# Kernel optimization log

Measured on AMD Instinct MI355X. Metric: run time of the kernel, lower is better.

Reference implementation:

```python
import jax, jax.numpy as jnp
import numpy as np

N = 100000
C = 20
D = 2001
REG = 0.001


def setup_inputs() -> dict:
    key = jax.random.key(0)
    k1, k2, k3, k4 = jax.random.split(key, 4)
    weights = jax.random.normal(k1, (C, D), dtype=jnp.float32)
    X = jax.random.normal(k2, (N, D), dtype=jnp.float32)
    Y = jax.random.randint(k3, (N,), 0, C, dtype=jnp.int64)
    init_weights = jax.random.uniform(k4, (C, D), dtype=jnp.float32)
    return {"weights": weights, "X": X, "Y": Y, "init_weights": init_weights}


def reference(weights, X, Y, init_weights):
    # scores[i, c] = X[i] . weights[c]  -> one batched GEMM [N,D]x[D,C]
    scores = jnp.einsum('nd,cd->nc', X, weights)
    # matmul(weights[Y[i]], X[i]) = scores[i, Y[i]]
    picked = jnp.take_along_axis(scores, Y[:, None].astype(jnp.int32), axis=1)[:, 0]  # [N]
    # logsumexp over classes of -X[i].weights (stable, single pass)
    lse = jax.nn.logsumexp(-scores, axis=1)  # [N]
    data_loss = jnp.mean(picked + lse)
    # torch.norm(self.weights, 2) on a matrix = Frobenius norm of init_weights (constant wrt input weights)
    reg = REG * jnp.sqrt(jnp.sum(init_weights * init_weights))
    return data_loss + reg
```

## Files before the change

kernel.cpp:

```cpp
#include <hip/hip_runtime.h>
#include <math.h>

#define DD 2001
#define CC 20
#define NN 100000
#define REGC 0.001f

__device__ __forceinline__ float4 ld4(const float* p) {
  return *reinterpret_cast<const float4*>(p);
}

template <int STRD, int STRC>
__global__ __launch_bounds__(64) void loss_main(
    const float* __restrict__ X,
    const float* __restrict__ Wp,
    const int* __restrict__ Y,
    float* __restrict__ out) {
  const float* W = (const float*)__builtin_assume_aligned(Wp, 64);
  const int lane = threadIdx.x;
  const int row0 = blockIdx.x * 64 + lane;
  const bool valid = row0 < NN;
  const int row = valid ? row0 : (NN - 1);
  const float* xr = X + (size_t)row * DD;

  float acc[CC];
#pragma unroll
  for (int c = 0; c < CC; ++c) acc[c] = 0.f;

  float4 c0 = ld4(xr), c1 = ld4(xr + 4), c2 = ld4(xr + 8), c3 = ld4(xr + 12);
#pragma unroll 1
  for (int k = 0; k < 125; ++k) {
    float4 n0 = {0, 0, 0, 0}, n1 = {0, 0, 0, 0}, n2 = {0, 0, 0, 0}, n3 = {0, 0, 0, 0};
    if (k < 124) {
      const float* p = xr + (k + 1) * 16;
      n0 = ld4(p); n1 = ld4(p + 4); n2 = ld4(p + 8); n3 = ld4(p + 12);
    }
    const int dbase = k * 16;
#pragma unroll
    for (int j = 0; j < 4; ++j) {
      const float4 x = (j == 0) ? c0 : (j == 1) ? c1 : (j == 2) ? c2 : c3;
      const int d0 = dbase + j * 4;
#pragma unroll
      for (int c = 0; c < CC; ++c) {
        float a = acc[c];
        a = fmaf(x.x, W[(d0 + 0) * STRD + c * STRC], a);
        a = fmaf(x.y, W[(d0 + 1) * STRD + c * STRC], a);
        a = fmaf(x.z, W[(d0 + 2) * STRD + c * STRC], a);
        a = fmaf(x.w, W[(d0 + 3) * STRD + c * STRC], a);
        acc[c] = a;
      }
    }
    c0 = n0; c1 = n1; c2 = n2; c3 = n3;
  }
  {
    const float x = xr[DD - 1];
#pragma unroll
    for (int c = 0; c < CC; ++c)
      acc[c] = fmaf(x, W[(DD - 1) * STRD + c * STRC], acc[c]);
  }

  float mx = -3.402823466e38f;
#pragma unroll
  for (int c = 0; c < CC; ++c) mx = fmaxf(mx, -acc[c]);
  float s = 0.f;
#pragma unroll
  for (int c = 0; c < CC; ++c) s += __expf(-acc[c] - mx);
  const int y = valid ? Y[row] : 0;
  float picked = 0.f;
#pragma unroll
  for (int c = 0; c < CC; ++c) picked = (c == y) ? acc[c] : picked;
  float li = picked + mx + __logf(s);
  li = valid ? li : 0.f;

#pragma unroll
  for (int off = 32; off > 0; off >>= 1) li += __shfl_xor(li, off, 64);
  if (lane == 0) atomicAdd(out, li * (1.0f / NN));
}

__global__ void reg_kernel(const float* __restrict__ IW, float* __restrict__ out) {
  __shared__ float red[256];
  float s = 0.f;
  for (int i = threadIdx.x; i < CC * DD; i += 256) {
    float v = IW[i];
    s += v * v;
  }
  red[threadIdx.x] = s;
  __syncthreads();
  for (int w = 128; w > 0; w >>= 1) {
    if (threadIdx.x < w) red[threadIdx.x] += red[threadIdx.x + w];
    __syncthreads();
  }
  if (threadIdx.x == 0) out[0] = REGC * sqrtf(red[0]);
}

__global__ void transpose_w(const float* __restrict__ W, float* __restrict__ Wt) {
  int i = blockIdx.x * 256 + threadIdx.x;
  if (i < CC * DD) {
    int c = i / DD;
    int d = i - c * DD;
    Wt[d * CC + c] = W[i];
  }
}

extern "C" void kernel_launch(void* const* d_in, const int* in_sizes, int n_in,
                              void* d_out, int out_size, void* d_ws, size_t ws_size,
                              hipStream_t stream) {
  const float* W  = (const float*)d_in[0];
  const float* X  = (const float*)d_in[1];
  const int*   Y  = (const int*)d_in[2];
  const float* IW = (const float*)d_in[3];
  float* out = (float*)d_out;

  reg_kernel<<<1, 256, 0, stream>>>(IW, out);

  const int nblocks = (NN + 63) / 64;
  if (ws_size >= (size_t)(CC * DD) * sizeof(float)) {
    float* Wt = (float*)d_ws;
    transpose_w<<<(CC * DD + 255) / 256, 256, 0, stream>>>(W, Wt);
    loss_main<CC, 1><<<nblocks, 64, 0, stream>>>(X, Wt, Y, out);
  } else {
    loss_main<1, DD><<<nblocks, 64, 0, stream>>>(X, W, Y, out);
  }
}
```

Measured before the change: 1.215 ms.

## Stage X tiles through LDS with coalesced loads and double-buffered registers

Each wavefront now loads 64-column chunks of its 64 rows cooperatively, with 16 lanes per row reading contiguous float4s. It writes them into a padded LDS tile so each lane can then read its own row's chunk for the per-class FMAs. The next chunk is prefetched into a second register buffer while the current one is consumed. The goal is to replace the old strided per-row global loads, which coalesced poorly, with coalesced transfers. The cost is LDS traffic, possible LDS hazards between write and read within the wave, and heavy register use from the 32 float4 buffers. The workspace-size fallback path is removed.

```diff
diff --git a/kernel.cpp b/kernel.cpp
--- a/kernel.cpp
+++ b/kernel.cpp
@@ -6,57 +6,88 @@
 #define NN 100000
 #define REGC 0.001f
 
+#define CH 64
+#define NFULL 31
+#define DTAIL 1984
+#define RSTR 68
+
 __device__ __forceinline__ float4 ld4(const float* p) {
   return *reinterpret_cast<const float4*>(p);
 }
 
-template <int STRD, int STRC>
 __global__ __launch_bounds__(64) void loss_main(
     const float* __restrict__ X,
-    const float* __restrict__ Wp,
+    const float* __restrict__ Wt,
     const int* __restrict__ Y,
     float* __restrict__ out) {
-  const float* W = (const float*)__builtin_assume_aligned(Wp, 64);
+  __shared__ float xs[64 * RSTR];
   const int lane = threadIdx.x;
-  const int row0 = blockIdx.x * 64 + lane;
-  const bool valid = row0 < NN;
-  const int row = valid ? row0 : (NN - 1);
-  const float* xr = X + (size_t)row * DD;
+  const int rowbase = blockIdx.x * 64;
+
+  const int myrow0 = rowbase + lane;
+  const bool valid = myrow0 < NN;
+  const int myrow = valid ? myrow0 : NN - 1;
+
+  const int srow = lane >> 4;
+  const int sf   = lane & 15;
 
   float acc[CC];
 #pragma unroll
   for (int c = 0; c < CC; ++c) acc[c] = 0.f;
 
-  float4 c0 = ld4(xr), c1 = ld4(xr + 4), c2 = ld4(xr + 8), c3 = ld4(xr + 12);
-#pragma unroll 1
-  for (int k = 0; k < 125; ++k) {
-    float4 n0 = {0, 0, 0, 0}, n1 = {0, 0, 0, 0}, n2 = {0, 0, 0, 0}, n3 = {0, 0, 0, 0};
-    if (k < 124) {
-      const float* p = xr + (k + 1) * 16;
-      n0 = ld4(p); n1 = ld4(p + 4); n2 = ld4(p + 8); n3 = ld4(p + 12);
+  float4 va[16], vb[16];
+
+  size_t sbase[16];
+#pragma unroll
+  for (int q = 0; q < 16; ++q) {
+    int r = rowbase + q * 4 + srow;
+    r = r < NN ? r : NN - 1;
+    sbase[q] = (size_t)r * DD + sf * 4;
+  }
+
+#pragma unroll
+  for (int q = 0; q < 16; ++q) va[q] = ld4(X + sbase[q]);
+
+  auto body = [&](float4 (&cur)[16], float4 (&nxt)[16], int k) {
+#pragma unroll
+    for (int q = 0; q < 16; ++q)
+      *reinterpret_cast<float4*>(&xs[(q * 4 + srow) * RSTR + sf * 4]) = cur[q];
+    if (k + 1 < NFULL) {
+#pragma unroll
+      for (int q = 0; q < 16; ++q)
+        nxt[q] = ld4(X + sbase[q] + (size_t)(k + 1) * CH);
     }
-    const int dbase = k * 16;
+    const int dbase = k * CH;
 #pragma unroll
-    for (int j = 0; j < 4; ++j) {
-      const float4 x = (j == 0) ? c0 : (j == 1) ? c1 : (j == 2) ? c2 : c3;
-      const int d0 = dbase + j * 4;
+    for (int f = 0; f < 16; ++f) {
+      float4 x4 = *reinterpret_cast<const float4*>(&xs[lane * RSTR + f * 4]);
+      const float xv[4] = {x4.x, x4.y, x4.z, x4.w};
 #pragma unroll
-      for (int c = 0; c < CC; ++c) {
-        float a = acc[c];
-        a = fmaf(x.x, W[(d0 + 0) * STRD + c * STRC], a);
-        a = fmaf(x.y, W[(d0 + 1) * STRD + c * STRC], a);
-        a = fmaf(x.z, W[(d0 + 2) * STRD + c * STRC], a);
-        a = fmaf(x.w, W[(d0 + 3) * STRD + c * STRC], a);
-        acc[c] = a;
+      for (int j = 0; j < 4; ++j) {
+        const int d = dbase + f * 4 + j;
+        const float xx = xv[j];
+#pragma unroll
+        for (int c = 0; c < CC; ++c)
+          acc[c] = fmaf(xx, Wt[d * CC + c], acc[c]);
       }
     }
-    c0 = n0; c1 = n1; c2 = n2; c3 = n3;
+  };
+
+  for (int k = 0; k < NFULL - 1; k += 2) {
+    body(va, vb, k);
+    body(vb, va, k + 1);
   }
+  body(va, vb, NFULL - 1);
+
   {
-    const float x = xr[DD - 1];
+    const float* xr = X + (size_t)myrow * DD;
 #pragma unroll
-    for (int c = 0; c < CC; ++c)
-      acc[c] = fmaf(x, W[(DD - 1) * STRD + c * STRC], acc[c]);
+    for (int d = DTAIL; d < DD; ++d) {
+      const float xx = xr[d];
+#pragma unroll
+      for (int c = 0; c < CC; ++c)
+        acc[c] = fmaf(xx, Wt[d * CC + c], acc[c]);
+    }
   }
 
   float mx = -3.402823466e38f;
@@ -65,7 +96,7 @@
   float s = 0.f;
 #pragma unroll
   for (int c = 0; c < CC; ++c) s += __expf(-acc[c] - mx);
-  const int y = valid ? Y[row] : 0;
+  const int y = valid ? Y[myrow] : 0;
   float picked = 0.f;
 #pragma unroll
   for (int c = 0; c < CC; ++c) picked = (c == y) ? acc[c] : picked;
@@ -113,12 +144,9 @@
 
   reg_kernel<<<1, 256, 0, stream>>>(IW, out);
 
+  float* Wt = (float*)d_ws;
+  transpose_w<<<(CC * DD + 255) / 256, 256, 0, stream>>>(W, Wt);
+
   const int nblocks = (NN + 63) / 64;
-  if (ws_size >= (size_t)(CC * DD) * sizeof(float)) {
-    float* Wt = (float*)d_ws;
-    transpose_w<<<(CC * DD + 255) / 256, 256, 0, stream>>>(W, Wt);
-    loss_main<CC, 1><<<nblocks, 64, 0, stream>>>(X, Wt, Y, out);
-  } else {
-    loss_main<1, DD><<<nblocks, 64, 0, stream>>>(X, W, Y, out);
-  }
+  loss_main<<<nblocks, 64, 0, stream>>>(X, Wt, Y, out);
 }
```

New measurement: 1.353 ms. 11.4% more time.

## Split D across slices with LDS-staged tiles and separate logsumexp epilogue

Applied to the files above, without the earlier changes.

Splits the reduction dimension into four slices per row group, giving four times more blocks. X and transposed W chunks are staged through shared memory with prefetching, and per-slice partial scores are written to a workspace. A new epilogue kernel sums the partials, computes logsumexp and the picked score, and does one atomic per block. This adds partial-score traffic and drops the small-workspace fallback.

```diff
diff --git a/kernel.cpp b/kernel.cpp
--- a/kernel.cpp
+++ b/kernel.cpp
@@ -6,75 +6,153 @@
 #define NN 100000
 #define REGC 0.001f
 
+#define NSLICE 4
+#define NRG 1563
+
+#define PART_BYTES ((size_t)NSLICE * CC * NN * 4)
+
 __device__ __forceinline__ float4 ld4(const float* p) {
   return *reinterpret_cast<const float4*>(p);
 }
 
-template <int STRD, int STRC>
-__global__ __launch_bounds__(64) void loss_main(
+__global__ __launch_bounds__(64, 4) void loss_partial(
     const float* __restrict__ X,
-    const float* __restrict__ Wp,
+    const float* __restrict__ Wt,
+    float* __restrict__ part) {
+  __shared__ float xs[64 * 20];
+  __shared__ float wc[16 * 20];
+  const int lane = threadIdx.x;
+  const int rg = blockIdx.x;
+  const int slice = blockIdx.y;
+  const int rowbase = rg * 64;
+  const int row0 = rowbase + lane;
+  const bool valid = row0 < NN;
+
+  const int ch0 = (slice == 0) ? 0 : (32 + 31 * (slice - 1));
+  const int nch = (slice == 0) ? 32 : 31;
+
+  const int srow = lane >> 2;
+  const int sf = lane & 3;
+  unsigned sb[4];
+#pragma unroll
+  for (int q = 0; q < 4; ++q) {
+    int r = rowbase + q * 16 + srow;
+    r = r < NN ? r : NN - 1;
+    sb[q] = (unsigned)r * DD + sf * 4u;
+  }
+
+  float acc[CC];
+#pragma unroll
+  for (int c = 0; c < CC; ++c) acc[c] = 0.f;
+
+  float4 xa[4];
+  float4 wa0, wa1;
+  {
+    const unsigned doff = (unsigned)ch0 * 16u;
+#pragma unroll
+    for (int q = 0; q < 4; ++q) xa[q] = ld4(X + sb[q] + doff);
+    const float* wp = Wt + (size_t)ch0 * (16 * CC);
+    wa0 = ld4(wp + lane * 4);
+    wa1 = (lane < 16) ? ld4(wp + 256 + lane * 4)
+                      : float4{0, 0, 0, 0};
+  }
+
+#pragma unroll 1
+  for (int ch = 0; ch < nch; ++ch) {
+#pragma unroll
+    for (int q = 0; q < 4; ++q)
+      *reinterpret_cast<float4*>(&xs[(q * 16 + srow) * 20 + sf * 4]) = xa[q];
+    *reinterpret_cast<float4*>(&wc[lane * 4]) = wa0;
+    if (lane < 16) *reinterpret_cast<float4*>(&wc[256 + lane * 4]) = wa1;
+
+    if (ch + 1 < nch) {
+      const unsigned doff = (unsigned)(ch0 + ch + 1) * 16u;
+#pragma unroll
+      for (int q = 0; q < 4; ++q) xa[q] = ld4(X + sb[q] + doff);
+      const float* wp = Wt + (size_t)(ch0 + ch + 1) * (16 * CC);
+      wa0 = ld4(wp + lane * 4);
+      if (lane < 16) wa1 = ld4(wp + 256 + lane * 4);
+    }
+
+#pragma unroll
+    for (int f = 0; f < 4; ++f) {
+      const float4 xv = *reinterpret_cast<const float4*>(&xs[lane * 20 + f * 4]);
+      const float xj[4] = {xv.x, xv.y, xv.z, xv.w};
+#pragma unroll
+      for (int j = 0; j < 4; ++j) {
+        const int d = f * 4 + j;
+        const float xx = xj[j];
+        const float4 w0 = *reinterpret_cast<const float4*>(&wc[d * 20 + 0]);
+        const float4 w1 = *reinterpret_cast<const float4*>(&wc[d * 20 + 4]);
+        const float4 w2 = *reinterpret_cast<const float4*>(&wc[d * 20 + 8]);
+        const float4 w3 = *reinterpret_cast<const float4*>(&wc[d * 20 + 12]);
+        const float4 w4 = *reinterpret_cast<const float4*>(&wc[d * 20 + 16]);
+        acc[0] = fmaf(xx, w0.x, acc[0]);   acc[1] = fmaf(xx, w0.y, acc[1]);
+        acc[2] = fmaf(xx, w0.z, acc[2]);   acc[3] = fmaf(xx, w0.w, acc[3]);
+        acc[4] = fmaf(xx, w1.x, acc[4]);   acc[5] = fmaf(xx, w1.y, acc[5]);
+        acc[6] = fmaf(xx, w1.z, acc[6]);   acc[7] = fmaf(xx, w1.w, acc[7]);
+        acc[8] = fmaf(xx, w2.x, acc[8]);   acc[9] = fmaf(xx, w2.y, acc[9]);
+        acc[10] = fmaf(xx, w2.z, acc[10]); acc[11] = fmaf(xx, w2.w, acc[11]);
+        acc[12] = fmaf(xx, w3.x, acc[12]); acc[13] = fmaf(xx, w3.y, acc[13]);
+        acc[14] = fmaf(xx, w3.z, acc[14]); acc[15] = fmaf(xx, w3.w, acc[15]);
+        acc[16] = fmaf(xx, w4.x, acc[16]); acc[17] = fmaf(xx, w4.y, acc[17]);
+        acc[18] = fmaf(xx, w4.z, acc[18]); acc[19] = fmaf(xx, w4.w, acc[19]);
+      }
+    }
+  }
+
+  if (slice == NSLICE - 1) {
+    const int r = valid ? row0 : NN - 1;
+    const float xx = X[(size_t)r * DD + 2000];
+#pragma unroll
+    for (int c = 0; c < CC; ++c)
+      acc[c] = fmaf(xx, Wt[2000 * CC + c], acc[c]);
+  }
+
+  if (valid) {
+    float* pb = part + (size_t)slice * CC * NN + row0;
+#pragma unroll
+    for (int c = 0; c < CC; ++c) pb[(size_t)c * NN] = acc[c];
+  }
+}
+
+__global__ __launch_bounds__(256) void loss_epilogue(
+    const float* __restrict__ part,
     const int* __restrict__ Y,
     float* __restrict__ out) {
-  const float* W = (const float*)__builtin_assume_aligned(Wp, 64);
-  const int lane = threadIdx.x;
-  const int row0 = blockIdx.x * 64 + lane;
-  const bool valid = row0 < NN;
-  const int row = valid ? row0 : (NN - 1);
-  const float* xr = X + (size_t)row * DD;
-
-  float acc[CC];
-#pragma unroll
-  for (int c = 0; c < CC; ++c) acc[c] = 0.f;
-
-  float4 c0 = ld4(xr), c1 = ld4(xr + 4), c2 = ld4(xr + 8), c3 = ld4(xr + 12);
-#pragma unroll 1
-  for (int k = 0; k < 125; ++k) {
-    float4 n0 = {0, 0, 0, 0}, n1 = {0, 0, 0, 0}, n2 = {0, 0, 0, 0}, n3 = {0, 0, 0, 0};
-    if (k < 124) {
-      const float* p = xr + (k + 1) * 16;
-      n0 = ld4(p); n1 = ld4(p + 4); n2 = ld4(p + 8); n3 = ld4(p + 12);
-    }
-    const int dbase = k * 16;
-#pragma unroll
-    for (int j = 0; j < 4; ++j) {
-      const float4 x = (j == 0) ? c0 : (j == 1) ? c1 : (j == 2) ? c2 : c3;
-      const int d0 = dbase + j * 4;
-#pragma unroll
-      for (int c = 0; c < CC; ++c) {
-        float a = acc[c];
-        a = fmaf(x.x, W[(d0 + 0) * STRD + c * STRC], a);
-        a = fmaf(x.y, W[(d0 + 1) * STRD + c * STRC], a);
-        a = fmaf(x.z, W[(d0 + 2) * STRD + c * STRC], a);
-        a = fmaf(x.w, W[(d0 + 3) * STRD + c * STRC], a);
-        acc[c] = a;
-      }
-    }
-    c0 = n0; c1 = n1; c2 = n2; c3 = n3;
-  }
-  {
-    const float x = xr[DD - 1];
-#pragma unroll
-    for (int c = 0; c < CC; ++c)
-      acc[c] = fmaf(x, W[(DD - 1) * STRD + c * STRC], acc[c]);
+  const int i = blockIdx.x * 256 + threadIdx.x;
+  const bool valid = i < NN;
+  const int row = valid ? i : NN - 1;
+
+  float sc[CC];
+#pragma unroll
+  for (int c = 0; c < CC; ++c) {
+    float s = 0.f;
+#pragma unroll
+    for (int sl = 0; sl < NSLICE; ++sl)
+      s += part[((size_t)(sl * CC + c)) * NN + row];
+    sc[c] = s;
   }
 
   float mx = -3.402823466e38f;
 #pragma unroll
-  for (int c = 0; c < CC; ++c) mx = fmaxf(mx, -acc[c]);
-  float s = 0.f;
-#pragma unroll
-  for (int c = 0; c < CC; ++c) s += __expf(-acc[c] - mx);
+  for (int c = 0; c < CC; ++c) mx = fmaxf(mx, -sc[c]);
+  float se = 0.f;
+#pragma unroll
+  for (int c = 0; c < CC; ++c) se += __expf(-sc[c] - mx);
   const int y = valid ? Y[row] : 0;
   float picked = 0.f;
 #pragma unroll
-  for (int c = 0; c < CC; ++c) picked = (c == y) ? acc[c] : picked;
-  float li = picked + mx + __logf(s);
-  li = valid ? li : 0.f;
+  for (int c = 0; c < CC; ++c) picked = (c == y) ? sc[c] : picked;
+  float li = valid ? (picked + mx + __logf(se)) : 0.f;
 
 #pragma unroll
   for (int off = 32; off > 0; off >>= 1) li += __shfl_xor(li, off, 64);
-  if (lane == 0) atomicAdd(out, li * (1.0f / NN));
+  __shared__ float red[4];
+  if ((threadIdx.x & 63) == 0) red[threadIdx.x >> 6] = li;
+  __syncthreads();
+  if (threadIdx.x == 0)
+    atomicAdd(out, (red[0] + red[1] + red[2] + red[3]) * (1.0f / NN));
 }
 
 __global__ void reg_kernel(const float* __restrict__ IW, float* __restrict__ out) {
@@ -111,14 +189,12 @@
   const float* IW = (const float*)d_in[3];
   float* out = (float*)d_out;
 
+  float* part = (float*)d_ws;
+  float* Wt = (float*)((char*)d_ws + PART_BYTES);
+
   reg_kernel<<<1, 256, 0, stream>>>(IW, out);
-
-  const int nblocks = (NN + 63) / 64;
-  if (ws_size >= (size_t)(CC * DD) * sizeof(float)) {
-    float* Wt = (float*)d_ws;
-    transpose_w<<<(CC * DD + 255) / 256, 256, 0, stream>>>(W, Wt);
-    loss_main<CC, 1><<<nblocks, 64, 0, stream>>>(X, Wt, Y, out);
-  } else {
-    loss_main<1, DD><<<nblocks, 64, 0, stream>>>(X, W, Y, out);
-  }
-}
+  transpose_w<<<(CC * DD + 255) / 256, 256, 0, stream>>>(W, Wt);
+  dim3 grid(NRG, NSLICE);
+  loss_partial<<<grid, 64, 0, stream>>>(X, Wt, part);
+  loss_epilogue<<<(NN + 255) / 256, 256, 0, stream>>>(part, Y, out);
+}
```

After: 1.146 ms. -5.7%, faster.
